# Performance work log

Measured on AMD Instinct MI355X. Metric: run time of the kernel, lower is better.

## Reference

```python
import jax, jax.numpy as jnp
import numpy as np

L = 40   # seq_length (sentence includes root; sent_length = L-1)
B = 16   # batch
V = 10000  # vocab
F = 512  # feature_size = 2*hidden (bidirectional)
H = 256  # classifier hidden
NEG = -jnp.inf


def _mlp(x, W1, b1, W2, b2):
    # Classifier / BinaryClassifier: Linear -> tanh -> Linear
    return jnp.tanh(x @ W1 + b1) @ W2 + b2


def setup_inputs() -> dict:
    key = jax.random.key(0)
    ks = jax.random.split(key, 10)
    s = 0.05
    return {
        "h": jax.random.normal(ks[0], (L, B, F), jnp.float32),
        "sentence": jax.random.randint(ks[1], (L, B), 0, V),
        "Wt1": jax.random.normal(ks[2], (2 * F, H), jnp.float32) * s,
        "bt1": jnp.zeros((H,), jnp.float32),
        "Wt2": jax.random.normal(ks[3], (H, 1), jnp.float32) * s,
        "bt2": jnp.zeros((1,), jnp.float32),
        "Ww1": jax.random.normal(ks[4], (2 * F, H), jnp.float32) * s,
        "bw1": jnp.zeros((H,), jnp.float32),
        "Ww2": jax.random.normal(ks[5], (H, V), jnp.float32) * s,
        "bw2": jnp.zeros((V,), jnp.float32),
    }


def reference(h, sentence, Wt1, bt1, Wt2, bt2, Ww1, bw1, Ww2, bw2):
    sent_length = L - 1
    # all ordered pairs i < j (forward enumeration order of batch_feature_selection)
    iu, ju = np.triu_indices(L, k=1)          # [P]
    feat = jnp.concatenate([h[iu], h[ju]], axis=-1)   # [P, B, 2F]

    t_logit = _mlp(feat, Wt1, bt1, Wt2, bt2)[..., 0]  # [P, B]
    sh = jax.nn.log_sigmoid(-t_logit)                 # shift log-prob
    re = jax.nn.log_sigmoid(t_logit)                  # reduce log-prob

    # word model log-softmax, gathered at target token sentence[j+1]
    wl = _mlp(feat, Ww1, bw1, Ww2, bw2)               # [P, B, V]
    ju1 = np.minimum(ju + 1, L - 1)                   # pairs with j = L-1 are unused
    tgt = sentence[ju1]                               # [P, B]
    gathered = jnp.take_along_axis(wl, tgt[..., None], axis=-1)[..., 0]
    wlp = gathered - jax.nn.logsumexp(wl, axis=-1)    # [P, B]

    # dense [L, L, B] tables (only i<j entries used)
    SHW = jnp.full((L, L, B), NEG, jnp.float32).at[iu, ju].set(sh + wlp)  # word_prob_list
    RE = jnp.full((L, L, B), NEG, jnp.float32).at[iu, ju].set(re)

    # init cell: stack_next=False -> word prob of sentence[1] from features (0,0)
    feat0 = jnp.concatenate([h[0], h[0]], axis=-1)    # [B, 2F]
    lp0 = jax.nn.log_softmax(_mlp(feat0, Ww1, bw1, Ww2, bw2), axis=-1)
    init = jnp.take_along_axis(lp0, sentence[1][:, None], axis=1)[:, 0]  # [B]

    T = jnp.full((L, L, B), NEG, jnp.float32)
    T = T.at[0, 1].set(init)
    T = T.at[jnp.arange(1, sent_length), jnp.arange(2, sent_length + 1)].set(0.0)

    # CKY-style DP over span widths; each width is vectorized over start i and split k
    for gap in range(2, sent_length + 1):
        n_i = sent_length + 1 - gap
        i_arr = np.arange(n_i)
        j_arr = i_arr + gap
        k = i_arr[:, None] + np.arange(1, gap)[None, :]   # [n_i, gap-1]
        scores = (T[i_arr[:, None], k] + T[k, j_arr[:, None]]
                  + SHW[i_arr[:, None], k] + RE[k, j_arr[:, None]])  # [n_i, gap-1, B]
        T = T.at[i_arr, j_arr].set(jax.nn.logsumexp(scores, axis=1))

    # stack_next=False -> final_score = 0
    return T[0, sent_length]
```

## Files before the change

### kernel.cpp

```cpp
#include <hip/hip_runtime.h>
#include <hip/hip_bf16.h>

#define L_SEQ 40
#define B_SZ  16
#define V_SZ  10000
#define V_PAD 10240
#define NPAIR 780
#define NROWP 784
#define M_ROWS (NROWP * B_SZ)

typedef __attribute__((ext_vector_type(4))) float f32x4;
typedef __attribute__((ext_vector_type(4))) int   i32x4;
typedef __attribute__((ext_vector_type(8))) int   i32x8;

#if __has_builtin(__builtin_amdgcn_cvt_pk_fp8_f32)
__device__ __forceinline__ unsigned int pack4_fp8(float x0, float x1, float x2, float x3) {
    int lo = __builtin_amdgcn_cvt_pk_fp8_f32(x0, x1, 0, false);
    int full = __builtin_amdgcn_cvt_pk_fp8_f32(x2, x3, lo, true);
    return (unsigned int)full;
}
#else
__device__ __forceinline__ unsigned char f2e4m3(float f) {
    unsigned u = __float_as_uint(f);
    unsigned s = (u >> 24) & 0x80u;
    if ((u & 0x7FFFFFFFu) == 0) return (unsigned char)s;
    int E = (int)((u >> 23) & 0xFF) - 127 + 7;
    unsigned m = u & 0x7FFFFFu;
    if (E >= 16) return (unsigned char)(s | 0x7E);
    if (E >= 1) {
        unsigned keep = m >> 20, rest = m & 0xFFFFFu;
        keep += (rest > 0x80000u) || (rest == 0x80000u && (keep & 1));
        if (keep == 8) { keep = 0; E++; if (E >= 16) return (unsigned char)(s | 0x7E); }
        return (unsigned char)(s | (E << 3) | keep);
    }
    int shift = 1 - E;
    if (shift > 10) return (unsigned char)s;
    unsigned full = 0x800000u | m;
    unsigned sh = 20 + shift;
    unsigned keep = full >> sh, rem = full & ((1u << sh) - 1), half = 1u << (sh - 1);
    keep += (rem > half) || (rem == half && (keep & 1));
    if (keep >= 8) return (unsigned char)(s | (1 << 3));
    return (unsigned char)(s | keep);
}
__device__ __forceinline__ unsigned int pack4_fp8(float x0, float x1, float x2, float x3) {
    return (unsigned int)f2e4m3(x0) | ((unsigned int)f2e4m3(x1) << 8)
         | ((unsigned int)f2e4m3(x2) << 16) | ((unsigned int)f2e4m3(x3) << 24);
}
#endif

#if __has_builtin(__builtin_amdgcn_exp2f)
__device__ __forceinline__ float exp2_hw(float x) { return __builtin_amdgcn_exp2f(x); }
#else
__device__ __forceinline__ float exp2_hw(float x) { return __expf(x * 0.6931471805599453f); }
#endif

#if __has_builtin(__builtin_amdgcn_rcpf)
__device__ __forceinline__ float rcp_hw(float x) { return __builtin_amdgcn_rcpf(x); }
#else
__device__ __forceinline__ float rcp_hw(float x) { return 1.0f / x; }
#endif

__device__ __forceinline__ float fast_tanh(float x) {
    float e = exp2_hw(x * 2.885390081777926814f);
    return fmaf(-2.0f, rcp_hw(e + 1.0f), 1.0f);
}


__global__ __launch_bounds__(256) void prep_kernel(
        const float* __restrict__ Ww2, float* __restrict__ WwT,
        unsigned char* __restrict__ WbT,
        const float* __restrict__ h, const float* __restrict__ Wt1,
        const float* __restrict__ Ww1, float* __restrict__ UV,
        float* __restrict__ rowsum) {
    const int bx = blockIdx.x;
    const int t = threadIdx.x;
    __shared__ float tile[32][33];
    __shared__ float hs[8 * 512];
    if (bx < 2560) {
        int v0 = (bx % 320) * 32;
        int K8 = bx / 320;
        int k0 = K8 * 32;
        int tx = t & 31, ty = t >> 5;
#pragma unroll
        for (int r = 0; r < 4; r++) {
            int k = k0 + ty + r * 8;
            int v = v0 + tx;
            tile[ty + r * 8][tx] = (v < V_SZ) ? Ww2[k * V_SZ + v] : 0.0f;
        }
        __syncthreads();
#pragma unroll
        for (int r = 0; r < 4; r++) {
            int vrow = ty + r * 8;
            WwT[(v0 + vrow) * 256 + (k0 + tx)] = tile[tx][vrow];
        }
        int v2 = t >> 3;
        int kq = 4 * (t & 7);
        unsigned int pk = pack4_fp8(tile[kq][v2], tile[kq + 1][v2],
                                    tile[kq + 2][v2], tile[kq + 3][v2]);
        ((unsigned int*)WbT)[(v0 + v2) * 64 + K8 * 8 + (t & 7)] = pk;
    } else if (bx < 2880) {
        int ub = bx - 2560;
        int which = ub / 80;
        int m0 = (ub % 80) * 8;
        const float4* src = (const float4*)(h + (size_t)m0 * 512);
        float4* dst4 = (float4*)hs;
#pragma unroll
        for (int v = 0; v < 4; v++) dst4[v * 256 + t] = src[v * 256 + t];
        __syncthreads();
        const float* W = ((which < 2) ? Wt1 : Ww1) + ((which & 1) ? 512 * 256 : 0);
        float acc[8] = {};
        for (int f = 0; f < 512; f += 4) {
            float w0 = W[(f + 0) * 256 + t];
            float w1 = W[(f + 1) * 256 + t];
            float w2 = W[(f + 2) * 256 + t];
            float w3 = W[(f + 3) * 256 + t];
#pragma unroll
            for (int r = 0; r < 8; r++) {
                acc[r] += hs[r * 512 + f] * w0 + hs[r * 512 + f + 1] * w1
                        + hs[r * 512 + f + 2] * w2 + hs[r * 512 + f + 3] * w3;
            }
        }
        float* dst = UV + ((size_t)which * 640 + m0) * 256;
#pragma unroll
        for (int r = 0; r < 8; r++) dst[r * 256 + t] = acc[r];
    } else {
        int idx = (bx - 2880) * 256 + t;
        if (idx < M_ROWS) rowsum[idx] = 0.0f;
    }
}

__global__ void build_rows(const float* __restrict__ UV,
                           const int* __restrict__ sentence,
                           const float* __restrict__ bt1,
                           const float* __restrict__ bw1,
                           const float* __restrict__ Wt2,
                           const float* __restrict__ bt2,
                           const float* __restrict__ WwT,
                           const float* __restrict__ bw2,
                           unsigned char* __restrict__ X,
                           float* __restrict__ tlog,
                           float* __restrict__ glog) {
    int w = blockIdx.x * 4 + (threadIdx.x >> 6);
    int lane = threadIdx.x & 63;
    int p = w >> 4, b = w & 15;
    int i = 0, j = 0;
    if (p < NPAIR) {
        int rem = p, len = L_SEQ - 1;
        while (rem >= len) { rem -= len; len--; i++; }
        j = i + 1 + rem;
    }
    int j1 = (j + 1 < L_SEQ) ? j + 1 : L_SEQ - 1;
    int tgt = sentence[j1 * B_SZ + b];
    const float4 ut = ((const float4*)(UV + 0 * 640 * 256 + (i * B_SZ + b) * 256))[lane];
    const float4 vt = ((const float4*)(UV + 1 * 640 * 256 + (j * B_SZ + b) * 256))[lane];
    const float4 uw = ((const float4*)(UV + 2 * 640 * 256 + (i * B_SZ + b) * 256))[lane];
    const float4 vw = ((const float4*)(UV + 3 * 640 * 256 + (j * B_SZ + b) * 256))[lane];
    const float4 bt = ((const float4*)bt1)[lane];
    const float4 bw = ((const float4*)bw1)[lane];
    const float4 w2 = ((const float4*)Wt2)[lane];
    const float4 wc = ((const float4*)(WwT + (size_t)tgt * 256))[lane];
    float xt0 = fast_tanh(ut.x + vt.x + bt.x), xt1 = fast_tanh(ut.y + vt.y + bt.y);
    float xt2 = fast_tanh(ut.z + vt.z + bt.z), xt3 = fast_tanh(ut.w + vt.w + bt.w);
    float xw0 = fast_tanh(uw.x + vw.x + bw.x), xw1 = fast_tanh(uw.y + vw.y + bw.y);
    float xw2 = fast_tanh(uw.z + vw.z + bw.z), xw3 = fast_tanh(uw.w + vw.w + bw.w);
    ((unsigned int*)X)[w * 64 + lane] = pack4_fp8(xw0, xw1, xw2, xw3);
    float td = xt0 * w2.x + xt1 * w2.y + xt2 * w2.z + xt3 * w2.w;
    float gd = xw0 * wc.x + xw1 * wc.y + xw2 * wc.z + xw3 * wc.w;
#pragma unroll
    for (int off = 32; off >= 1; off >>= 1) {
        td += __shfl_xor(td, off);
        gd += __shfl_xor(gd, off);
    }
    if (lane == 0) {
        tlog[w] = td + bt2[0];
        glog[w] = gd + bw2[tgt];
    }
}

__global__ __launch_bounds__(256, 3) void big_gemm(
        const unsigned char* __restrict__ X,
        const unsigned char* __restrict__ WbT,
        const float* __restrict__ bw2,
        float* __restrict__ rowsum) {
    __shared__ unsigned char Bs[3][64 * 256];
    const int t = threadIdx.x;
    const int wid = t >> 6, lane = t & 63;
    const int l15 = lane & 15, l4 = lane >> 4;
    const int g = blockIdx.x;
    const int row0 = blockIdx.y * 128 + wid * 32;
    const int NIT = 20;

    auto dmaB = [&](int buf, int it) {
        const unsigned char* Bg = WbT + (size_t)(g * 1280 + it * 64) * 256;
#pragma unroll
        for (int q = 0; q < 4; q++) {
            int off = (wid * 4 + q) * 1024;
            int F = off + lane * 16;
            int cc = F >> 8;
            int s = (F >> 4) & 15;
            int srcg = s ^ (cc & 15);
            __builtin_amdgcn_global_load_lds(
                (const __attribute__((address_space(1))) unsigned int*)(Bg + cc * 256 + (srcg << 4)),
                (__attribute__((address_space(3))) unsigned int*)(&Bs[buf][0] + off),
                16, 0, 0);
        }
    };

    i32x8 apan[2][2];
    {
        const unsigned char* Ag = X + (size_t)row0 * 256;
#pragma unroll
        for (int mi = 0; mi < 2; mi++)
#pragma unroll
            for (int kb = 0; kb < 2; kb++)
                apan[mi][kb] = *(const i32x8*)(Ag + (mi * 16 + l15) * 256 + kb * 128 + l4 * 32);
    }
    dmaB(0, 0);
    dmaB(1, 1);

    float PS[2][4] = {};
    const float L2E = 1.44269504088896340736f;
    int cur = 0, pre = 2;

#pragma unroll 1
    for (int it = 0; it < NIT; it++) {
        if (it < NIT - 1) {
            asm volatile("s_waitcnt vmcnt(4)\n\ts_barrier" ::: "memory");
        } else {
            asm volatile("s_waitcnt vmcnt(0)\n\ts_barrier" ::: "memory");
        }
        if (it + 2 < NIT) dmaB(pre, it + 2);
        const unsigned char* Bb = &Bs[cur][0];
        f32x4 acc[2][4] = {};
#pragma unroll
        for (int kb = 0; kb < 2; kb++) {
#pragma unroll
            for (int ni = 0; ni < 4; ni++) {
                int cc = ni * 16 + l15;
                int g0 = kb * 8 + l4 * 2;
                i32x4 lo = *(const i32x4*)(Bb + cc * 256 + (((g0 + 0) ^ (cc & 15)) << 4));
                i32x4 hi = *(const i32x4*)(Bb + cc * 256 + (((g0 + 1) ^ (cc & 15)) << 4));
                i32x8 bv = {lo.x, lo.y, lo.z, lo.w, hi.x, hi.y, hi.z, hi.w};
                acc[0][ni] = __builtin_amdgcn_mfma_scale_f32_16x16x128_f8f6f4(
                    apan[0][kb], bv, acc[0][ni], 0, 0,
                    0, 0x7F7F7F7F, 0, 0x7F7F7F7F);
                acc[1][ni] = __builtin_amdgcn_mfma_scale_f32_16x16x128_f8f6f4(
                    apan[1][kb], bv, acc[1][ni], 0, 0,
                    0, 0x7F7F7F7F, 0, 0x7F7F7F7F);
            }
        }
#pragma unroll
        for (int ni = 0; ni < 4; ni++) {
            int col = g * 1280 + it * 64 + ni * 16 + l15;
            float bL = (col < V_SZ) ? bw2[col] * L2E : -__builtin_inff();
#pragma unroll
            for (int mi = 0; mi < 2; mi++)
#pragma unroll
                for (int r = 0; r < 4; r++)
                    PS[mi][r] += exp2_hw(fmaf(acc[mi][ni][r], L2E, bL));
        }
        cur = (cur == 2) ? 0 : cur + 1;
        pre = (pre == 2) ? 0 : pre + 1;
    }
#pragma unroll
    for (int mi = 0; mi < 2; mi++)
#pragma unroll
        for (int r = 0; r < 4; r++) {
            float v = PS[mi][r];
            v += __shfl_xor(v, 1); v += __shfl_xor(v, 2);
            v += __shfl_xor(v, 4); v += __shfl_xor(v, 8);
            if (l15 == 0)
                atomicAdd(&rowsum[row0 + mi * 16 + l4 * 4 + r], v);
        }
}

__global__ __launch_bounds__(1024) void dp_kernel(const float* __restrict__ tlog,
                          const float* __restrict__ glog,
                          const float* __restrict__ rowsum,
                          float* __restrict__ out) {
    __shared__ float Tl[1600], SHWl[1600], REl[1600];
    const int t = threadIdx.x;
    const int b = blockIdx.x;
    const float NEGINF = -__builtin_inff();
    for (int idx = t; idx < 1600; idx += 1024) {
        Tl[idx] = NEGINF; SHWl[idx] = NEGINF; REl[idx] = NEGINF;
    }
    __syncthreads();
    for (int p = t; p < NPAIR; p += 1024) {
        int i = 0, rem = p, len = L_SEQ - 1;
        while (rem >= len) { rem -= len; len--; i++; }
        int j = i + 1 + rem;
        int row = p * 16 + b;
        float tl = tlog[row];
        float re_v = (tl >= 0.f) ? -log1pf(__expf(-tl)) : (tl - log1pf(__expf(tl)));
        float sh_v = (tl <= 0.f) ? -log1pf(__expf(tl)) : (-tl - log1pf(__expf(-tl)));
        float wlp = glog[row] - __logf(rowsum[row]);
        SHWl[i * 40 + j] = sh_v + wlp;
        REl[i * 40 + j] = re_v;
    }
    if (t == 0) {
        int row = NPAIR * 16 + b;
        Tl[0 * 40 + 1] = glog[row] - __logf(rowsum[row]);
    }
    if (t >= 1 && t <= 38) Tl[t * 40 + t + 1] = 0.f;
    __syncthreads();
    const int tg = t >> 4, li = t & 15;
    for (int gap = 2; gap <= L_SEQ - 1; gap++) {
        int n_i = L_SEQ - gap;
        float m = NEGINF, s = 0.f;
        int i = tg, j = tg + gap;
        if (tg < n_i) {
            for (int k = i + 1 + li; k < j; k += 16) {
                float v = Tl[i * 40 + k] + Tl[k * 40 + j]
                        + SHWl[i * 40 + k] + REl[k * 40 + j];
                if (v > m) { s = s * __expf(m - v) + 1.f; m = v; }
                else s += __expf(v - m);
            }
        }
#pragma unroll
        for (int off = 1; off < 16; off <<= 1) {
            float mo = __shfl_xor(m, off), so = __shfl_xor(s, off);
            float M = fmaxf(m, mo);
            float sn = 0.f;
            if (m > NEGINF) sn += s * __expf(m - M);
            if (mo > NEGINF) sn += so * __expf(mo - M);
            m = M; s = sn;
        }
        if (tg < n_i && li == 0) Tl[i * 40 + j] = m + __logf(s);
        __syncthreads();
    }
    if (t == 0) out[b] = Tl[39];
}

extern "C" void kernel_launch(void* const* d_in, const int* in_sizes, int n_in,
                              void* d_out, int out_size, void* d_ws, size_t ws_size,
                              hipStream_t stream) {
    const float* h        = (const float*)d_in[0];
    const int*   sentence = (const int*)d_in[1];
    const float* Wt1      = (const float*)d_in[2];
    const float* bt1      = (const float*)d_in[3];
    const float* Wt2      = (const float*)d_in[4];
    const float* bt2      = (const float*)d_in[5];
    const float* Ww1      = (const float*)d_in[6];
    const float* bw1      = (const float*)d_in[7];
    const float* Ww2      = (const float*)d_in[8];
    const float* bw2      = (const float*)d_in[9];
    float* out = (float*)d_out;

    char* ws = (char*)d_ws;
    size_t off = 0;
    float* UV = (float*)(ws + off);                    off += 4ull * 640 * 256 * 4;
    unsigned char* X = (unsigned char*)(ws + off);     off += (size_t)M_ROWS * 256;
    unsigned char* WbT = (unsigned char*)(ws + off);   off += (size_t)V_PAD * 256;
    float* WwT = (float*)(ws + off);                   off += (size_t)V_PAD * 256 * 4;
    float* rowsum = (float*)(ws + off);                off += (size_t)M_ROWS * 4;
    float* tlog = (float*)(ws + off);                  off += (size_t)M_ROWS * 4;
    float* glog = (float*)(ws + off);                  off += (size_t)M_ROWS * 4;

    const int zero_blocks = (M_ROWS + 255) / 256;
    prep_kernel<<<2880 + zero_blocks, 256, 0, stream>>>(
        Ww2, WwT, WbT, h, Wt1, Ww1, UV, rowsum);
    build_rows<<<M_ROWS / 4, 256, 0, stream>>>(UV, sentence, bt1, bw1, Wt2, bt2,
                                               WwT, bw2, X, tlog, glog);
    big_gemm<<<dim3(8, 98), 256, 0, stream>>>(X, WbT, bw2, rowsum);
    dp_kernel<<<16, 1024, 0, stream>>>(tlog, glog, rowsum, out);
}
```

Baseline: 217.3 us.

## Software-pipeline LDS B-fragment reads with MFMA and precompute bias in shared memory

Restructures the big_gemm inner loop so LDS reads of B fragments are double-buffered in registers and interleaved with the MFMA issues, including prefetching the next tile's first quarter before the current tile finishes. Bias values scaled by log2(e) are precomputed once per block into shared memory instead of being loaded from global memory each iteration, and swizzled LDS offsets are precomputed. The DMA issue now comes before the wait and barrier, and an explicit __syncthreads covers the bias table. This adds register pressure from the extra fragment buffers and offset array, under a 3-blocks-per-CU launch bound. It also relies on the barrier ordering being correct for the triple-buffered LDS.

```diff
diff --git a/kernel.cpp b/kernel.cpp
--- a/kernel.cpp
+++ b/kernel.cpp
@@ -177,18 +177,61 @@
     }
 }
 
+#define RDQ(BASE, Q, BR) \
+    BR[0] = *(const i32x4*)((BASE) + offs[(Q)*4+0]); \
+    BR[1] = *(const i32x4*)((BASE) + offs[(Q)*4+1]); \
+    BR[2] = *(const i32x4*)((BASE) + offs[(Q)*4+2]); \
+    BR[3] = *(const i32x4*)((BASE) + offs[(Q)*4+3]);
+
+#define MFQ(Q, BR) { \
+    i32x8 bv0_ = __builtin_shufflevector(BR[0], BR[1], 0,1,2,3,4,5,6,7); \
+    acc[0][((Q)&1)*2] = __builtin_amdgcn_mfma_scale_f32_16x16x128_f8f6f4( \
+        apan[0][(Q)>>1], bv0_, acc[0][((Q)&1)*2], 0,0, 0,0x7F7F7F7F, 0,0x7F7F7F7F); \
+    acc[1][((Q)&1)*2] = __builtin_amdgcn_mfma_scale_f32_16x16x128_f8f6f4( \
+        apan[1][(Q)>>1], bv0_, acc[1][((Q)&1)*2], 0,0, 0,0x7F7F7F7F, 0,0x7F7F7F7F); \
+    i32x8 bv1_ = __builtin_shufflevector(BR[2], BR[3], 0,1,2,3,4,5,6,7); \
+    acc[0][((Q)&1)*2+1] = __builtin_amdgcn_mfma_scale_f32_16x16x128_f8f6f4( \
+        apan[0][(Q)>>1], bv1_, acc[0][((Q)&1)*2+1], 0,0, 0,0x7F7F7F7F, 0,0x7F7F7F7F); \
+    acc[1][((Q)&1)*2+1] = __builtin_amdgcn_mfma_scale_f32_16x16x128_f8f6f4( \
+        apan[1][(Q)>>1], bv1_, acc[1][((Q)&1)*2+1], 0,0, 0,0x7F7F7F7F, 0,0x7F7F7F7F); \
+}
+
 __global__ __launch_bounds__(256, 3) void big_gemm(
         const unsigned char* __restrict__ X,
         const unsigned char* __restrict__ WbT,
         const float* __restrict__ bw2,
         float* __restrict__ rowsum) {
     __shared__ unsigned char Bs[3][64 * 256];
+    __shared__ float biasL[1280];
     const int t = threadIdx.x;
     const int wid = t >> 6, lane = t & 63;
     const int l15 = lane & 15, l4 = lane >> 4;
     const int g = blockIdx.x;
     const int row0 = blockIdx.y * 128 + wid * 32;
     const int NIT = 20;
+    const float L2E = 1.44269504088896340736f;
+
+#pragma unroll
+    for (int k = 0; k < 5; k++) {
+        int idx = k * 256 + t;
+        int col = g * 1280 + idx;
+        biasL[idx] = (col < V_SZ) ? bw2[col] * L2E : -__builtin_inff();
+    }
+
+    int offs[16];
+#pragma unroll
+    for (int q = 0; q < 4; q++) {
+        int kb = q >> 1, np = q & 1;
+#pragma unroll
+        for (int nn = 0; nn < 2; nn++)
+#pragma unroll
+            for (int gg = 0; gg < 2; gg++) {
+                int ni = np * 2 + nn;
+                int cc = ni * 16 + l15;
+                int gr = kb * 8 + l4 * 2 + gg;
+                offs[q * 4 + nn * 2 + gg] = cc * 256 + ((gr ^ (cc & 15)) << 4);
+            }
+    }
 
     auto dmaB = [&](int buf, int it) {
         const unsigned char* Bg = WbT + (size_t)(g * 1280 + it * 64) * 256;
@@ -206,6 +249,7 @@
         }
     };
 
+    dmaB(0, 0);
     i32x8 apan[2][2];
     {
         const unsigned char* Ag = X + (size_t)row0 * 256;
@@ -215,52 +259,43 @@
             for (int kb = 0; kb < 2; kb++)
                 apan[mi][kb] = *(const i32x8*)(Ag + (mi * 16 + l15) * 256 + kb * 128 + l4 * 32);
     }
-    dmaB(0, 0);
     dmaB(1, 1);
+    __syncthreads();
+
+    i32x4 br0[4], br1[4];
+    RDQ(&Bs[0][0], 0, br0);
 
     float PS[2][4] = {};
-    const float L2E = 1.44269504088896340736f;
-    int cur = 0, pre = 2;
 
 #pragma unroll 1
     for (int it = 0; it < NIT; it++) {
-        if (it < NIT - 1) {
-            asm volatile("s_waitcnt vmcnt(4)\n\ts_barrier" ::: "memory");
+        if (it + 2 < NIT) dmaB((it + 2) % 3, it + 2);
+        if (it < NIT - 2) {
+            asm volatile("s_waitcnt vmcnt(4)" ::: "memory");
         } else {
-            asm volatile("s_waitcnt vmcnt(0)\n\ts_barrier" ::: "memory");
-        }
-        if (it + 2 < NIT) dmaB(pre, it + 2);
-        const unsigned char* Bb = &Bs[cur][0];
+            asm volatile("s_waitcnt vmcnt(0)" ::: "memory");
+        }
+        __builtin_amdgcn_s_barrier();
+        const unsigned char* bufC = &Bs[it % 3][0];
+        const unsigned char* bufN = &Bs[(it + 1) % 3][0];
+        float bl[4];
+#pragma unroll
+        for (int ni = 0; ni < 4; ni++) bl[ni] = biasL[it * 64 + ni * 16 + l15];
         f32x4 acc[2][4] = {};
-#pragma unroll
-        for (int kb = 0; kb < 2; kb++) {
-#pragma unroll
-            for (int ni = 0; ni < 4; ni++) {
-                int cc = ni * 16 + l15;
-                int g0 = kb * 8 + l4 * 2;
-                i32x4 lo = *(const i32x4*)(Bb + cc * 256 + (((g0 + 0) ^ (cc & 15)) << 4));
-                i32x4 hi = *(const i32x4*)(Bb + cc * 256 + (((g0 + 1) ^ (cc & 15)) << 4));
-                i32x8 bv = {lo.x, lo.y, lo.z, lo.w, hi.x, hi.y, hi.z, hi.w};
-                acc[0][ni] = __builtin_amdgcn_mfma_scale_f32_16x16x128_f8f6f4(
-                    apan[0][kb], bv, acc[0][ni], 0, 0,
-                    0, 0x7F7F7F7F, 0, 0x7F7F7F7F);
-                acc[1][ni] = __builtin_amdgcn_mfma_scale_f32_16x16x128_f8f6f4(
-                    apan[1][kb], bv, acc[1][ni], 0, 0,
-                    0, 0x7F7F7F7F, 0, 0x7F7F7F7F);
-            }
-        }
+        RDQ(bufC, 1, br1); MFQ(0, br0);
+        RDQ(bufC, 2, br0); MFQ(1, br1);
+        RDQ(bufC, 3, br1); MFQ(2, br0);
+        if (it + 1 < NIT) { RDQ(bufN, 0, br0); }
+        MFQ(3, br1);
 #pragma unroll
         for (int ni = 0; ni < 4; ni++) {
-            int col = g * 1280 + it * 64 + ni * 16 + l15;
-            float bL = (col < V_SZ) ? bw2[col] * L2E : -__builtin_inff();
+            float bL = bl[ni];
 #pragma unroll
             for (int mi = 0; mi < 2; mi++)
 #pragma unroll
                 for (int r = 0; r < 4; r++)
                     PS[mi][r] += exp2_hw(fmaf(acc[mi][ni][r], L2E, bL));
         }
-        cur = (cur == 2) ? 0 : cur + 1;
-        pre = (pre == 2) ? 0 : pre + 1;
     }
 #pragma unroll
     for (int mi = 0; mi < 2; mi++)
```

Measured after the change: 209.2 us. 1.04x faster.
